# Performance work log

Measured on AMD Instinct MI355X. Metric: run time of the kernel, lower is better.

The kernel has to match this reference:

```python
import jax, jax.numpy as jnp
import numpy as np

N_HEADS = 16
D_MODEL = 1024
D_HEAD = D_MODEL // N_HEADS


def setup_inputs() -> dict:
    key = jax.random.key(0)
    k1, k2, k3, k4, k5 = jax.random.split(key, 5)
    B, S = 4, 2048
    scale = 1.0 / np.sqrt(D_MODEL)
    return {
        "x": jax.random.normal(k1, (B, S, D_MODEL), dtype=jnp.float32),
        "W_in": jax.random.normal(k2, (3 * D_MODEL, D_MODEL), dtype=jnp.float32) * scale,
        "b_in": jax.random.normal(k3, (3 * D_MODEL,), dtype=jnp.float32) * 0.02,
        "W_out": jax.random.normal(k4, (D_MODEL, D_MODEL), dtype=jnp.float32) * scale,
        "b_out": jax.random.normal(k5, (D_MODEL,), dtype=jnp.float32) * 0.02,
        "causal_mask": 1,
    }


def reference(x, W_in, b_in, W_out, b_out, causal_mask):
    b, s, d = x.shape
    # in_proj: torch Linear -> x @ W.T + b, then chunk into q,k,v
    qkv = jnp.einsum("bsd,ed->bse", x, W_in) + b_in
    q, k, v = jnp.split(qkv, 3, axis=-1)
    # [b, s, h, dh] -> [b, h, s, dh]
    q = q.reshape(b, s, N_HEADS, D_HEAD).transpose(0, 2, 1, 3)
    k = k.reshape(b, s, N_HEADS, D_HEAD).transpose(0, 2, 1, 3)
    v = v.reshape(b, s, N_HEADS, D_HEAD).transpose(0, 2, 1, 3)
    # scores [b, h, s, s]
    qk = jnp.einsum("bhqd,bhkd->bhqk", q, k)
    if causal_mask:
        mask = jnp.triu(jnp.ones((s, s), dtype=bool), k=1)
        qk = jnp.where(mask, -jnp.inf, qk)
    qk = qk / jnp.sqrt(jnp.float32(D_HEAD))
    attn = jax.nn.softmax(qk, axis=-1)
    out = jnp.einsum("bhqk,bhkd->bhqd", attn, v)  # [b, h, s, dh]
    out = out.transpose(0, 2, 1, 3).reshape(b, s, d)
    return jnp.einsum("bsd,ed->bse", out, W_out) + b_out
```

## Files before the change

### kernel.cpp

```cpp
#include <hip/hip_runtime.h>
#include <hip/hip_bf16.h>
#include <cstdint>
#include <cstddef>

typedef short bf16x8 __attribute__((ext_vector_type(8)));
typedef float f32x4 __attribute__((ext_vector_type(4)));

#define SEQ 2048
#define NH 16
#define DH 64
#define DM 1024

typedef __attribute__((address_space(1))) const void gvoid_t;
typedef __attribute__((address_space(3))) void lvoid_t;

__device__ __forceinline__ unsigned short f2bf(float f) {
  union { float f; unsigned int u; } v; v.f = f;
  return (unsigned short)((v.u + 0x7FFFu + ((v.u >> 16) & 1u)) >> 16);
}

__global__ void __launch_bounds__(256) k_cvt3(const float* __restrict__ x,
                                              const float* __restrict__ wi,
                                              const float* __restrict__ wo,
                                              unsigned short* __restrict__ xb,
                                              unsigned short* __restrict__ wib,
                                              unsigned short* __restrict__ wob) {
  int bidx = blockIdx.x;
  const float* src; unsigned short* dst; int base;
  if (bidx < 8192)       { src = x;  dst = xb;  base = bidx; }
  else if (bidx < 11264) { src = wi; dst = wib; base = bidx - 8192; }
  else                   { src = wo; dst = wob; base = bidx - 11264; }
  int i = (base * 256 + threadIdx.x) * 4;
  float4 v = *(const float4*)(src + i);
  ushort4 o;
  o.x = f2bf(v.x); o.y = f2bf(v.y); o.z = f2bf(v.z); o.w = f2bf(v.w);
  *(ushort4*)(dst + i) = o;
}

#define LDS_T 16384

__device__ __forceinline__ void barx() {
  asm volatile("" ::: "memory");
  __builtin_amdgcn_s_barrier();
  asm volatile("" ::: "memory");
}
#define LGKM0() asm volatile("s_waitcnt lgkmcnt(0)" ::: "memory")
#define VMC4()  asm volatile("s_waitcnt vmcnt(4)" ::: "memory")

__device__ __forceinline__ void stage_half(const unsigned short* __restrict__ G,
                                           int row0, int kt, unsigned short* lds,
                                           int Rhalf, int rstat, int cOff, int wave) {
#pragma unroll
  for (int pc = 0; pc < 2; ++pc) {
    const int R = Rhalf + pc * 64;
    __builtin_amdgcn_global_load_lds(
        (gvoid_t*)(G + (size_t)(row0 + R + rstat) * DM + kt * 64 + cOff),
        (lvoid_t*)(lds + (R + wave * 8) * 64), 16, 0, 0);
  }
}

__device__ __forceinline__ void lda8(const unsigned short* lds, int rb, int l16,
                                     int sw0, int sw1, bf16x8 (&a)[8]) {
#pragma unroll
  for (int f = 0; f < 4; ++f) {
    const unsigned short* p = lds + (rb + f * 16 + l16) * 64;
    a[f * 2 + 0] = *(const bf16x8*)(p + sw0);
    a[f * 2 + 1] = *(const bf16x8*)(p + sw1);
  }
}

__device__ __forceinline__ void ldb4(const unsigned short* lds, int rb, int l16,
                                     int sw0, int sw1, bf16x8 (&b)[4]) {
#pragma unroll
  for (int g = 0; g < 2; ++g) {
    const unsigned short* p = lds + (rb + g * 16 + l16) * 64;
    b[g * 2 + 0] = *(const bf16x8*)(p + sw0);
    b[g * 2 + 1] = *(const bf16x8*)(p + sw1);
  }
}

template <int MQ, int NQ>
__device__ __forceinline__ void mfma_quad(const bf16x8 (&a)[8], const bf16x8 (&b)[4],
                                          f32x4 (&acc)[8][4]) {
  __builtin_amdgcn_s_setprio(1);
#pragma unroll
  for (int f = 0; f < 4; ++f)
#pragma unroll
    for (int g = 0; g < 2; ++g) {
      f32x4 c = acc[MQ * 4 + f][NQ * 2 + g];
      c = __builtin_amdgcn_mfma_f32_16x16x32_bf16(a[f * 2 + 0], b[g * 2 + 0], c, 0, 0, 0);
      c = __builtin_amdgcn_mfma_f32_16x16x32_bf16(a[f * 2 + 1], b[g * 2 + 1], c, 0, 0, 0);
      acc[MQ * 4 + f][NQ * 2 + g] = c;
    }
  __builtin_amdgcn_s_setprio(0);
}

__device__ __forceinline__ void gemm256(const unsigned short* __restrict__ A,
                                        const unsigned short* __restrict__ Bt,
                                        unsigned short* lA, unsigned short* lB,
                                        int m0, int n0, f32x4 (&acc)[8][4]) {
  const int t = threadIdx.x;
  const int wave = t >> 6, lane = t & 63, quad = lane >> 4, l16 = lane & 15;
  const int wm = wave >> 2, wn = wave & 3;
  const int rstat = t >> 3;
  const int cOff = ((t & 7) ^ (rstat & 7)) * 8;
  const int sw0 = (quad ^ (l16 & 7)) * 8;
  const int sw1 = ((quad ^ 4) ^ (l16 & 7)) * 8;
  const int arb0 = wm * 64, arb1 = 128 + wm * 64;
  const int brb0 = wn * 32, brb1 = 128 + wn * 32;
  const int NT = DM / 64;

  bf16x8 af[8], b0[4], b1[4];

  stage_half(A,  m0, 0, lA, 0,   rstat, cOff, wave);
  stage_half(Bt, n0, 0, lB, 0,   rstat, cOff, wave);
  stage_half(A,  m0, 0, lA, 128, rstat, cOff, wave);
  stage_half(Bt, n0, 0, lB, 128, rstat, cOff, wave);
  stage_half(A,  m0, 1, lA + LDS_T, 0,   rstat, cOff, wave);
  stage_half(Bt, n0, 1, lB + LDS_T, 128, rstat, cOff, wave);
  VMC4();
  barx();

  for (int t0 = 0; t0 < NT; t0 += 2) {
    const int t2 = (t0 + 2 < NT) ? t0 + 2 : NT - 1;
    const int t3 = (t0 + 3 < NT) ? t0 + 3 : NT - 1;
    lda8(lA, arb0, l16, sw0, sw1, af);
    ldb4(lB, brb0, l16, sw0, sw1, b0);
    stage_half(A, m0, t0 + 1, lA + LDS_T, 128, rstat, cOff, wave);
    barx(); LGKM0();
    mfma_quad<0, 0>(af, b0, acc);
    barx();
    ldb4(lB, brb1, l16, sw0, sw1, b1);
    stage_half(Bt, n0, t0 + 1, lB + LDS_T, 0, rstat, cOff, wave);
    barx(); LGKM0();
    mfma_quad<0, 1>(af, b1, acc);
    barx();
    lda8(lA, arb1, l16, sw0, sw1, af);
    stage_half(A, m0, t2, lA, 0, rstat, cOff, wave);
    barx(); LGKM0();
    mfma_quad<1, 1>(af, b1, acc);
    barx();
    stage_half(Bt, n0, t2, lB, 128, rstat, cOff, wave);
    VMC4();
    barx(); LGKM0();
    mfma_quad<1, 0>(af, b0, acc);
    barx();
    lda8(lA + LDS_T, arb0, l16, sw0, sw1, af);
    ldb4(lB + LDS_T, brb0, l16, sw0, sw1, b0);
    stage_half(A, m0, t2, lA, 128, rstat, cOff, wave);
    barx(); LGKM0();
    mfma_quad<0, 0>(af, b0, acc);
    barx();
    ldb4(lB + LDS_T, brb1, l16, sw0, sw1, b1);
    stage_half(Bt, n0, t2, lB, 0, rstat, cOff, wave);
    barx(); LGKM0();
    mfma_quad<0, 1>(af, b1, acc);
    barx();
    lda8(lA + LDS_T, arb1, l16, sw0, sw1, af);
    stage_half(A, m0, t3, lA + LDS_T, 0, rstat, cOff, wave);
    barx(); LGKM0();
    mfma_quad<1, 1>(af, b1, acc);
    barx();
    stage_half(Bt, n0, t3, lB + LDS_T, 128, rstat, cOff, wave);
    VMC4();
    barx(); LGKM0();
    mfma_quad<1, 0>(af, b0, acc);
    barx();
  }
}

__global__ void __launch_bounds__(512, 2) k_gemm_qkv(
    const unsigned short* __restrict__ X,
    const unsigned short* __restrict__ Wi,
    const float* __restrict__ bias,
    unsigned short* __restrict__ Qo,
    unsigned short* __restrict__ Ko,
    unsigned short* __restrict__ Vto) {
  __shared__ unsigned short lA[2 * LDS_T];
  __shared__ unsigned short lB[2 * LDS_T];
  const int t = threadIdx.x;
  const int wave = t >> 6, lane = t & 63, quad = lane >> 4, l16 = lane & 15;
  const int wm = wave >> 2, wn = wave & 3;
  const int nwg = 32 * 12;
  const int bid = blockIdx.x;
  const int swz = (bid & 7) * (nwg / 8) + (bid >> 3);
  const int m0 = (swz / 12) * 256, n0 = (swz % 12) * 256;

  f32x4 acc[8][4];
  f32x4 zf = {0.f, 0.f, 0.f, 0.f};
#pragma unroll
  for (int i = 0; i < 8; ++i)
#pragma unroll
    for (int j = 0; j < 4; ++j) acc[i][j] = zf;

  gemm256(X, Wi, lA, lB, m0, n0, acc);

  const float SCALE = 0.18033688011112042f;
  const int sel = n0 >> 10;
#pragma unroll
  for (int nf = 0; nf < 4; ++nf) {
    const int gcol = n0 + (nf >> 1) * 128 + wn * 32 + (nf & 1) * 16 + l16;
    const float bv = bias[gcol];
    const int c = gcol & 1023;
    const int hh = c >> 6, dh = c & 63;
    if (sel == 0) {
#pragma unroll
      for (int mf = 0; mf < 8; ++mf) {
        const int grow = m0 + (mf >> 2) * 128 + wm * 64 + (mf & 3) * 16 + quad * 4;
        const int bb = grow >> 11, sb = grow & 2047;
        unsigned short* qp = Qo + ((size_t)(bb * NH + hh) * SEQ + sb) * DH + dh;
#pragma unroll
        for (int r = 0; r < 4; ++r)
          qp[(size_t)r * DH] = f2bf((acc[mf][nf][r] + bv) * SCALE);
      }
    } else if (sel == 1) {
#pragma unroll
      for (int mf = 0; mf < 8; ++mf) {
        const int grow = m0 + (mf >> 2) * 128 + wm * 64 + (mf & 3) * 16 + quad * 4;
        const int bb = grow >> 11, sb = grow & 2047;
        unsigned short* kp = Ko + ((size_t)(bb * NH + hh) * SEQ + sb) * DH + dh;
#pragma unroll
        for (int r = 0; r < 4; ++r)
          kp[(size_t)r * DH] = f2bf(acc[mf][nf][r] + bv);
      }
    } else {
#pragma unroll
      for (int mf = 0; mf < 8; ++mf) {
        const int grow = m0 + (mf >> 2) * 128 + wm * 64 + (mf & 3) * 16 + quad * 4;
        const int bb = grow >> 11, sb = grow & 2047;
        ushort4 pk;
        pk.x = f2bf(acc[mf][nf][0] + bv);
        pk.y = f2bf(acc[mf][nf][1] + bv);
        pk.z = f2bf(acc[mf][nf][2] + bv);
        pk.w = f2bf(acc[mf][nf][3] + bv);
        *(ushort4*)(&Vto[((size_t)(bb * NH + hh) * DH + dh) * SEQ + sb]) = pk;
      }
    }
  }
}

#define ASTR 72

__global__ void __launch_bounds__(256, 4) k_attn(
    const unsigned short* __restrict__ Q,
    const unsigned short* __restrict__ K,
    const unsigned short* __restrict__ Vt,
    unsigned short* __restrict__ Ao,
    const int* __restrict__ causal_p) {
  __shared__ unsigned short lK[64 * 64];
  __shared__ unsigned short lV[64 * 64];
  __shared__ unsigned short lP[2][4][16 * ASTR];

  const int t = threadIdx.x;
  const int wave = t >> 6, lane = t & 63, quad = lane >> 4, l16 = lane & 15;
  const int x = blockIdx.x, h = blockIdx.y, b = blockIdx.z;
  const int qtA = x, qtB = 31 - x;
  const int bh = b * NH + h;
  const int causal = causal_p[0];
  const int ktA = causal ? qtA : 31;
  const int ktB = causal ? qtB : 31;
  const int q0A = qtA * 64, q0B = qtB * 64;

  const unsigned short* Qb = Q + (size_t)bh * SEQ * DH;
  const unsigned short* Kb = K + (size_t)bh * SEQ * DH;
  const unsigned short* Vb = Vt + (size_t)bh * DH * SEQ;

  bf16x8 qA0 = *(const bf16x8*)(&Qb[(q0A + wave * 16 + l16) * DH + quad * 8]);
  bf16x8 qA1 = *(const bf16x8*)(&Qb[(q0A + wave * 16 + l16) * DH + 32 + quad * 8]);
  bf16x8 qB0 = *(const bf16x8*)(&Qb[(q0B + wave * 16 + l16) * DH + quad * 8]);
  bf16x8 qB1 = *(const bf16x8*)(&Qb[(q0B + wave * 16 + l16) * DH + 32 + quad * 8]);

  f32x4 zf = {0.f, 0.f, 0.f, 0.f};
  f32x4 oA[4], oB[4];
  for (int i = 0; i < 4; ++i) { oA[i] = zf; oB[i] = zf; }
  f32x4 lacA = zf, lacB = zf;

  bf16x8 ones;
#pragma unroll
  for (int i = 0; i < 8; ++i) ones[i] = (short)0x3F80;

  unsigned short* lPa = &lP[0][wave][0];
  unsigned short* lPb = &lP[1][wave][0];

  const int i0 = t, i1 = 256 + t;
  const int rr0 = i0 >> 3, cc0 = ((i0 & 7) ^ (rr0 & 7)) * 8;
  const int rr1 = i1 >> 3, cc1 = ((i1 & 7) ^ (rr1 & 7)) * 8;
  const int kof0 = rr0 * DH + cc0, kof1 = rr1 * DH + cc1;
  const int vof0 = rr0 * SEQ + cc0, vof1 = rr1 * SEQ + cc1;
  const int rbase = l16 * 64;
  const int sw0 = ((quad ^ (l16 & 7)) * 8);
  const int sw1 = (((quad ^ 4) ^ (l16 & 7)) * 8);

  for (int kt = 0; kt <= ktB; ++kt) {
    const int k0 = kt * 64;
    const bool doA = (kt <= ktA);

    __syncthreads();
    __builtin_amdgcn_global_load_lds((gvoid_t*)(Kb + (size_t)k0 * DH + kof0),
                                     (lvoid_t*)&lK[wave * 512], 16, 0, 0);
    __builtin_amdgcn_global_load_lds((gvoid_t*)(Kb + (size_t)k0 * DH + kof1),
                                     (lvoid_t*)&lK[wave * 512 + 2048], 16, 0, 0);
    __builtin_amdgcn_global_load_lds((gvoid_t*)(Vb + k0 + vof0),
                                     (lvoid_t*)&lV[wave * 512], 16, 0, 0);
    __builtin_amdgcn_global_load_lds((gvoid_t*)(Vb + k0 + vof1),
                                     (lvoid_t*)&lV[wave * 512 + 2048], 16, 0, 0);
    __syncthreads();

    f32x4 sA[4], sB[4];
#pragma unroll
    for (int nt = 0; nt < 4; ++nt) {
      bf16x8 kf0 = *(const bf16x8*)(&lK[nt * 1024 + rbase + sw0]);
      bf16x8 kf1 = *(const bf16x8*)(&lK[nt * 1024 + rbase + sw1]);
      f32x4 zb = zf;
      zb = __builtin_amdgcn_mfma_f32_16x16x32_bf16(qB0, kf0, zb, 0, 0, 0);
      zb = __builtin_amdgcn_mfma_f32_16x16x32_bf16(qB1, kf1, zb, 0, 0, 0);
      sB[nt] = zb;
      if (doA) {
        f32x4 za = zf;
        za = __builtin_amdgcn_mfma_f32_16x16x32_bf16(qA0, kf0, za, 0, 0, 0);
        za = __builtin_amdgcn_mfma_f32_16x16x32_bf16(qA1, kf1, za, 0, 0, 0);
        sA[nt] = za;
      }
    }

    if (causal && kt == qtB) {
#pragma unroll
      for (int nt = 0; nt < 4; ++nt) {
        int kcol = k0 + nt * 16 + l16;
#pragma unroll
        for (int r = 0; r < 4; ++r)
          if (kcol > q0B + wave * 16 + quad * 4 + r) sB[nt][r] = -1e30f;
      }
    }
    if (causal && doA && kt == qtA) {
#pragma unroll
      for (int nt = 0; nt < 4; ++nt) {
        int kcol = k0 + nt * 16 + l16;
#pragma unroll
        for (int r = 0; r < 4; ++r)
          if (kcol > q0A + wave * 16 + quad * 4 + r) sA[nt][r] = -1e30f;
      }
    }

#pragma unroll
    for (int nt = 0; nt < 4; ++nt)
#pragma unroll
      for (int r = 0; r < 4; ++r)
        lPb[(quad * 4 + r) * ASTR + nt * 16 + l16] =
            f2bf(__builtin_amdgcn_exp2f(sB[nt][r]));
    if (doA) {
#pragma unroll
      for (int nt = 0; nt < 4; ++nt)
#pragma unroll
        for (int r = 0; r < 4; ++r)
          lPa[(quad * 4 + r) * ASTR + nt * 16 + l16] =
              f2bf(__builtin_amdgcn_exp2f(sA[nt][r]));
    }

    asm volatile("s_waitcnt lgkmcnt(0)" ::: "memory");

    bf16x8 pB0 = *(const bf16x8*)(&lPb[l16 * ASTR + quad * 8]);
    bf16x8 pB1 = *(const bf16x8*)(&lPb[l16 * ASTR + 32 + quad * 8]);
    bf16x8 pA0 = pB0, pA1 = pB1;
    if (doA) {
      pA0 = *(const bf16x8*)(&lPa[l16 * ASTR + quad * 8]);
      pA1 = *(const bf16x8*)(&lPa[l16 * ASTR + 32 + quad * 8]);
    }

    lacB = __builtin_amdgcn_mfma_f32_16x16x32_bf16(pB0, ones, lacB, 0, 0, 0);
    lacB = __builtin_amdgcn_mfma_f32_16x16x32_bf16(pB1, ones, lacB, 0, 0, 0);
    if (doA) {
      lacA = __builtin_amdgcn_mfma_f32_16x16x32_bf16(pA0, ones, lacA, 0, 0, 0);
      lacA = __builtin_amdgcn_mfma_f32_16x16x32_bf16(pA1, ones, lacA, 0, 0, 0);
    }

#pragma unroll
    for (int nt = 0; nt < 4; ++nt) {
      bf16x8 vf0 = *(const bf16x8*)(&lV[nt * 1024 + rbase + sw0]);
      bf16x8 vf1 = *(const bf16x8*)(&lV[nt * 1024 + rbase + sw1]);
      oB[nt] = __builtin_amdgcn_mfma_f32_16x16x32_bf16(pB0, vf0, oB[nt], 0, 0, 0);
      oB[nt] = __builtin_amdgcn_mfma_f32_16x16x32_bf16(pB1, vf1, oB[nt], 0, 0, 0);
      if (doA) {
        oA[nt] = __builtin_amdgcn_mfma_f32_16x16x32_bf16(pA0, vf0, oA[nt], 0, 0, 0);
        oA[nt] = __builtin_amdgcn_mfma_f32_16x16x32_bf16(pA1, vf1, oA[nt], 0, 0, 0);
      }
    }
  }

#pragma unroll
  for (int r = 0; r < 4; ++r) {
    float invB = 1.0f / lacB[r];
    float invA = 1.0f / lacA[r];
#pragma unroll
    for (int nt = 0; nt < 4; ++nt) {
      int dh = nt * 16 + l16;
      int qgB = q0B + wave * 16 + quad * 4 + r;
      Ao[(size_t)(b * SEQ + qgB) * DM + h * DH + dh] = f2bf(oB[nt][r] * invB);
      int qgA = q0A + wave * 16 + quad * 4 + r;
      Ao[(size_t)(b * SEQ + qgA) * DM + h * DH + dh] = f2bf(oA[nt][r] * invA);
    }
  }
}

__global__ void __launch_bounds__(512, 2) k_gemm_out(
    const unsigned short* __restrict__ Ai,
    const unsigned short* __restrict__ Wo,
    const float* __restrict__ bias,
    float* __restrict__ C) {
  __shared__ unsigned short lA[2 * LDS_T];
  __shared__ unsigned short lB[2 * LDS_T];
  const int t = threadIdx.x;
  const int wave = t >> 6, lane = t & 63, quad = lane >> 4, l16 = lane & 15;
  const int wm = wave >> 2, wn = wave & 3;
  const int bid = blockIdx.x;
  const int swz = (bid & 7) * 16 + (bid >> 3);
  const int m0 = (swz >> 2) * 256, n0 = (swz & 3) * 256;

  f32x4 acc[8][4];
  f32x4 zf = {0.f, 0.f, 0.f, 0.f};
#pragma unroll
  for (int i = 0; i < 8; ++i)
#pragma unroll
    for (int j = 0; j < 4; ++j) acc[i][j] = zf;

  gemm256(Ai, Wo, lA, lB, m0, n0, acc);

#pragma unroll
  for (int nf = 0; nf < 4; ++nf) {
    const int gcol = n0 + (nf >> 1) * 128 + wn * 32 + (nf & 1) * 16 + l16;
    const float bv = bias[gcol];
#pragma unroll
    for (int mf = 0; mf < 8; ++mf) {
      const int grow = m0 + (mf >> 2) * 128 + wm * 64 + (mf & 3) * 16 + quad * 4;
#pragma unroll
      for (int r = 0; r < 4; ++r)
        C[(size_t)(grow + r) * DM + gcol] = acc[mf][nf][r] + bv;
    }
  }
}

extern "C" void kernel_launch(void* const* d_in, const int* in_sizes, int n_in,
                              void* d_out, int out_size, void* d_ws, size_t ws_size,
                              hipStream_t stream) {
  (void)in_sizes; (void)n_in; (void)out_size; (void)ws_size;
  const float* x     = (const float*)d_in[0];
  const float* W_in  = (const float*)d_in[1];
  const float* b_in  = (const float*)d_in[2];
  const float* W_out = (const float*)d_in[3];
  const float* b_out = (const float*)d_in[4];
  const int* causal  = (const int*)d_in[5];
  float* out = (float*)d_out;
  char* ws = (char*)d_ws;

  unsigned short* xb  = (unsigned short*)(ws + 0);
  unsigned short* Aob = (unsigned short*)(ws + 0);
  unsigned short* Wib = (unsigned short*)(ws + (size_t)(16 << 20));
  unsigned short* Wob = (unsigned short*)(ws + (size_t)(22 << 20));
  unsigned short* Qb  = (unsigned short*)(ws + (size_t)(24 << 20));
  unsigned short* Kb  = (unsigned short*)(ws + (size_t)(40 << 20));
  unsigned short* Vtb = (unsigned short*)(ws + (size_t)(56 << 20));

  k_cvt3<<<12288, 256, 0, stream>>>(x, W_in, W_out, xb, Wib, Wob);
  k_gemm_qkv<<<384, 512, 0, stream>>>(xb, Wib, b_in, Qb, Kb, Vtb);
  k_attn<<<dim3(16, 16, 4), 256, 0, stream>>>(Qb, Kb, Vtb, Aob, causal);
  k_gemm_out<<<128, 512, 0, stream>>>(Aob, Wob, b_out, out);
}
```

Baseline: 262.1 us.

## Double-buffer K/V tiles in attention and restructure GEMM staging with asm LDS reads

The attention kernel now double-buffers K and V tiles in LDS, prefetching the next tile with global_load_lds while the current one is computed. This replaces the two __syncthreads per iteration with a single vmcnt wait and barrier. The P buffer moves to a single XOR-swizzled per-wave layout written with ds_write_b16 and read with inline-asm ds_read_b128, so the A and B halves are processed in sequence through the same buffer. The GEMM mainloop reorders its staging sequence one half-tile earlier, uses vmcnt(6), adds sched_barrier fences around the MFMA blocks and switches LDS fragment reads to inline asm. The added explicit waits and scheduling fences risk serialising work the compiler could otherwise overlap.

```diff
diff --git a/kernel.cpp b/kernel.cpp
--- a/kernel.cpp
+++ b/kernel.cpp
@@ -13,11 +13,32 @@
 
 typedef __attribute__((address_space(1))) const void gvoid_t;
 typedef __attribute__((address_space(3))) void lvoid_t;
+typedef __attribute__((address_space(3))) const unsigned short ls_t;
 
 __device__ __forceinline__ unsigned short f2bf(float f) {
   union { float f; unsigned int u; } v; v.f = f;
   return (unsigned short)((v.u + 0x7FFFu + ((v.u >> 16) & 1u)) >> 16);
 }
+
+__device__ __forceinline__ bf16x8 dsr128(const unsigned short* p) {
+  bf16x8 r;
+  unsigned a = (unsigned)(size_t)(ls_t*)p;
+  asm volatile("ds_read_b128 %0, %1" : "=v"(r) : "v"(a));
+  return r;
+}
+__device__ __forceinline__ void dsw16(unsigned a, unsigned short v) {
+  asm volatile("ds_write_b16 %0, %1" :: "v"(a), "v"((unsigned)v));
+}
+
+__device__ __forceinline__ void barx() {
+  asm volatile("" ::: "memory");
+  __builtin_amdgcn_s_barrier();
+  asm volatile("" ::: "memory");
+}
+#define LGKM0() asm volatile("s_waitcnt lgkmcnt(0)" ::: "memory")
+#define VMC0()  asm volatile("s_waitcnt vmcnt(0)" ::: "memory")
+#define VMC6()  asm volatile("s_waitcnt vmcnt(6)" ::: "memory")
+#define SCHED0() __builtin_amdgcn_sched_barrier(0)
 
 __global__ void __launch_bounds__(256) k_cvt3(const float* __restrict__ x,
                                               const float* __restrict__ wi,
@@ -39,14 +60,6 @@
 
 #define LDS_T 16384
 
-__device__ __forceinline__ void barx() {
-  asm volatile("" ::: "memory");
-  __builtin_amdgcn_s_barrier();
-  asm volatile("" ::: "memory");
-}
-#define LGKM0() asm volatile("s_waitcnt lgkmcnt(0)" ::: "memory")
-#define VMC4()  asm volatile("s_waitcnt vmcnt(4)" ::: "memory")
-
 __device__ __forceinline__ void stage_half(const unsigned short* __restrict__ G,
                                            int row0, int kt, unsigned short* lds,
                                            int Rhalf, int rstat, int cOff, int wave) {
@@ -59,23 +72,23 @@
   }
 }
 
-__device__ __forceinline__ void lda8(const unsigned short* lds, int rb, int l16,
-                                     int sw0, int sw1, bf16x8 (&a)[8]) {
+__device__ __forceinline__ void lda8a(const unsigned short* lds, int rb, int l16,
+                                      int sw0, int sw1, bf16x8 (&a)[8]) {
 #pragma unroll
   for (int f = 0; f < 4; ++f) {
     const unsigned short* p = lds + (rb + f * 16 + l16) * 64;
-    a[f * 2 + 0] = *(const bf16x8*)(p + sw0);
-    a[f * 2 + 1] = *(const bf16x8*)(p + sw1);
-  }
-}
-
-__device__ __forceinline__ void ldb4(const unsigned short* lds, int rb, int l16,
-                                     int sw0, int sw1, bf16x8 (&b)[4]) {
+    a[f * 2 + 0] = dsr128(p + sw0);
+    a[f * 2 + 1] = dsr128(p + sw1);
+  }
+}
+
+__device__ __forceinline__ void ldb4a(const unsigned short* lds, int rb, int l16,
+                                      int sw0, int sw1, bf16x8 (&b)[4]) {
 #pragma unroll
   for (int g = 0; g < 2; ++g) {
     const unsigned short* p = lds + (rb + g * 16 + l16) * 64;
-    b[g * 2 + 0] = *(const bf16x8*)(p + sw0);
-    b[g * 2 + 1] = *(const bf16x8*)(p + sw1);
+    b[g * 2 + 0] = dsr128(p + sw0);
+    b[g * 2 + 1] = dsr128(p + sw1);
   }
 }
 
@@ -118,54 +131,55 @@
   stage_half(Bt, n0, 0, lB, 128, rstat, cOff, wave);
   stage_half(A,  m0, 1, lA + LDS_T, 0,   rstat, cOff, wave);
   stage_half(Bt, n0, 1, lB + LDS_T, 128, rstat, cOff, wave);
-  VMC4();
+  stage_half(A,  m0, 1, lA + LDS_T, 128, rstat, cOff, wave);
+  VMC6();
   barx();
 
   for (int t0 = 0; t0 < NT; t0 += 2) {
     const int t2 = (t0 + 2 < NT) ? t0 + 2 : NT - 1;
     const int t3 = (t0 + 3 < NT) ? t0 + 3 : NT - 1;
-    lda8(lA, arb0, l16, sw0, sw1, af);
-    ldb4(lB, brb0, l16, sw0, sw1, b0);
-    stage_half(A, m0, t0 + 1, lA + LDS_T, 128, rstat, cOff, wave);
-    barx(); LGKM0();
+    lda8a(lA, arb0, l16, sw0, sw1, af);
+    ldb4a(lB, brb0, l16, sw0, sw1, b0);
+    stage_half(Bt, n0, t0 + 1, lB + LDS_T, 0, rstat, cOff, wave);
+    barx(); LGKM0(); SCHED0();
     mfma_quad<0, 0>(af, b0, acc);
-    barx();
-    ldb4(lB, brb1, l16, sw0, sw1, b1);
-    stage_half(Bt, n0, t0 + 1, lB + LDS_T, 0, rstat, cOff, wave);
-    barx(); LGKM0();
+    SCHED0(); barx();
+    ldb4a(lB, brb1, l16, sw0, sw1, b1);
+    stage_half(A, m0, t2, lA, 0, rstat, cOff, wave);
+    barx(); LGKM0(); SCHED0();
     mfma_quad<0, 1>(af, b1, acc);
-    barx();
-    lda8(lA, arb1, l16, sw0, sw1, af);
-    stage_half(A, m0, t2, lA, 0, rstat, cOff, wave);
-    barx(); LGKM0();
+    SCHED0(); barx();
+    lda8a(lA, arb1, l16, sw0, sw1, af);
+    stage_half(Bt, n0, t2, lB, 128, rstat, cOff, wave);
+    barx(); LGKM0(); SCHED0();
     mfma_quad<1, 1>(af, b1, acc);
-    barx();
-    stage_half(Bt, n0, t2, lB, 128, rstat, cOff, wave);
-    VMC4();
-    barx(); LGKM0();
+    SCHED0(); barx();
+    stage_half(A, m0, t2, lA, 128, rstat, cOff, wave);
+    VMC6();
+    barx(); SCHED0();
     mfma_quad<1, 0>(af, b0, acc);
-    barx();
-    lda8(lA + LDS_T, arb0, l16, sw0, sw1, af);
-    ldb4(lB + LDS_T, brb0, l16, sw0, sw1, b0);
-    stage_half(A, m0, t2, lA, 128, rstat, cOff, wave);
-    barx(); LGKM0();
+    SCHED0(); barx();
+    lda8a(lA + LDS_T, arb0, l16, sw0, sw1, af);
+    ldb4a(lB + LDS_T, brb0, l16, sw0, sw1, b0);
+    stage_half(Bt, n0, t2, lB, 0, rstat, cOff, wave);
+    barx(); LGKM0(); SCHED0();
     mfma_quad<0, 0>(af, b0, acc);
-    barx();
-    ldb4(lB + LDS_T, brb1, l16, sw0, sw1, b1);
-    stage_half(Bt, n0, t2, lB, 0, rstat, cOff, wave);
-    barx(); LGKM0();
+    SCHED0(); barx();
+    ldb4a(lB + LDS_T, brb1, l16, sw0, sw1, b1);
+    stage_half(A, m0, t3, lA + LDS_T, 0, rstat, cOff, wave);
+    barx(); LGKM0(); SCHED0();
     mfma_quad<0, 1>(af, b1, acc);
-    barx();
-    lda8(lA + LDS_T, arb1, l16, sw0, sw1, af);
-    stage_half(A, m0, t3, lA + LDS_T, 0, rstat, cOff, wave);
-    barx(); LGKM0();
+    SCHED0(); barx();
+    lda8a(lA + LDS_T, arb1, l16, sw0, sw1, af);
+    stage_half(Bt, n0, t3, lB + LDS_T, 128, rstat, cOff, wave);
+    barx(); LGKM0(); SCHED0();
     mfma_quad<1, 1>(af, b1, acc);
-    barx();
-    stage_half(Bt, n0, t3, lB + LDS_T, 128, rstat, cOff, wave);
-    VMC4();
-    barx(); LGKM0();
+    SCHED0(); barx();
+    stage_half(A, m0, t3, lA + LDS_T, 128, rstat, cOff, wave);
+    VMC6();
+    barx(); SCHED0();
     mfma_quad<1, 0>(af, b0, acc);
-    barx();
+    SCHED0(); barx();
   }
 }
 
@@ -239,17 +253,15 @@
   }
 }
 
-#define ASTR 72
-
 __global__ void __launch_bounds__(256, 4) k_attn(
     const unsigned short* __restrict__ Q,
     const unsigned short* __restrict__ K,
     const unsigned short* __restrict__ Vt,
     unsigned short* __restrict__ Ao,
     const int* __restrict__ causal_p) {
-  __shared__ unsigned short lK[64 * 64];
-  __shared__ unsigned short lV[64 * 64];
-  __shared__ unsigned short lP[2][4][16 * ASTR];
+  __shared__ unsigned short lK[2][4096];
+  __shared__ unsigned short lV[2][4096];
+  __shared__ unsigned short lP[4][1024];
 
   const int t = threadIdx.x;
   const int wave = t >> 6, lane = t & 63, quad = lane >> 4, l16 = lane & 15;
@@ -279,8 +291,8 @@
 #pragma unroll
   for (int i = 0; i < 8; ++i) ones[i] = (short)0x3F80;
 
-  unsigned short* lPa = &lP[0][wave][0];
-  unsigned short* lPb = &lP[1][wave][0];
+  unsigned short* lPw = &lP[wave][0];
+  const unsigned pbase = (unsigned)(size_t)(ls_t*)lPw;
 
   const int i0 = t, i1 = 256 + t;
   const int rr0 = i0 >> 3, cc0 = ((i0 & 7) ^ (rr0 & 7)) * 8;
@@ -291,35 +303,56 @@
   const int sw0 = ((quad ^ (l16 & 7)) * 8);
   const int sw1 = (((quad ^ 4) ^ (l16 & 7)) * 8);
 
+  __builtin_amdgcn_global_load_lds((gvoid_t*)(Kb + kof0), (lvoid_t*)&lK[0][wave * 512], 16, 0, 0);
+  __builtin_amdgcn_global_load_lds((gvoid_t*)(Kb + kof1), (lvoid_t*)&lK[0][wave * 512 + 2048], 16, 0, 0);
+  __builtin_amdgcn_global_load_lds((gvoid_t*)(Vb + vof0), (lvoid_t*)&lV[0][wave * 512], 16, 0, 0);
+  __builtin_amdgcn_global_load_lds((gvoid_t*)(Vb + vof1), (lvoid_t*)&lV[0][wave * 512 + 2048], 16, 0, 0);
+
   for (int kt = 0; kt <= ktB; ++kt) {
+    const int cur = kt & 1;
     const int k0 = kt * 64;
     const bool doA = (kt <= ktA);
 
-    __syncthreads();
-    __builtin_amdgcn_global_load_lds((gvoid_t*)(Kb + (size_t)k0 * DH + kof0),
-                                     (lvoid_t*)&lK[wave * 512], 16, 0, 0);
-    __builtin_amdgcn_global_load_lds((gvoid_t*)(Kb + (size_t)k0 * DH + kof1),
-                                     (lvoid_t*)&lK[wave * 512 + 2048], 16, 0, 0);
-    __builtin_amdgcn_global_load_lds((gvoid_t*)(Vb + k0 + vof0),
-                                     (lvoid_t*)&lV[wave * 512], 16, 0, 0);
-    __builtin_amdgcn_global_load_lds((gvoid_t*)(Vb + k0 + vof1),
-                                     (lvoid_t*)&lV[wave * 512 + 2048], 16, 0, 0);
-    __syncthreads();
+    VMC0();
+    barx();
+    if (kt < ktB) {
+      const int kn = k0 + 64;
+      __builtin_amdgcn_global_load_lds((gvoid_t*)(Kb + (size_t)kn * DH + kof0),
+                                       (lvoid_t*)&lK[cur ^ 1][wave * 512], 16, 0, 0);
+      __builtin_amdgcn_global_load_lds((gvoid_t*)(Kb + (size_t)kn * DH + kof1),
+                                       (lvoid_t*)&lK[cur ^ 1][wave * 512 + 2048], 16, 0, 0);
+      __builtin_amdgcn_global_load_lds((gvoid_t*)(Vb + kn + vof0),
+                                       (lvoid_t*)&lV[cur ^ 1][wave * 512], 16, 0, 0);
+      __builtin_amdgcn_global_load_lds((gvoid_t*)(Vb + kn + vof1),
+                                       (lvoid_t*)&lV[cur ^ 1][wave * 512 + 2048], 16, 0, 0);
+    }
+    const unsigned short* lk = &lK[cur][0];
+    const unsigned short* lv = &lV[cur][0];
 
     f32x4 sA[4], sB[4];
 #pragma unroll
-    for (int nt = 0; nt < 4; ++nt) {
-      bf16x8 kf0 = *(const bf16x8*)(&lK[nt * 1024 + rbase + sw0]);
-      bf16x8 kf1 = *(const bf16x8*)(&lK[nt * 1024 + rbase + sw1]);
-      f32x4 zb = zf;
-      zb = __builtin_amdgcn_mfma_f32_16x16x32_bf16(qB0, kf0, zb, 0, 0, 0);
-      zb = __builtin_amdgcn_mfma_f32_16x16x32_bf16(qB1, kf1, zb, 0, 0, 0);
-      sB[nt] = zb;
-      if (doA) {
-        f32x4 za = zf;
-        za = __builtin_amdgcn_mfma_f32_16x16x32_bf16(qA0, kf0, za, 0, 0, 0);
-        za = __builtin_amdgcn_mfma_f32_16x16x32_bf16(qA1, kf1, za, 0, 0, 0);
-        sA[nt] = za;
+    for (int g = 0; g < 2; ++g) {
+      bf16x8 kf[4];
+#pragma unroll
+      for (int j = 0; j < 2; ++j) {
+        const unsigned short* p = lk + (g * 2 + j) * 1024 + rbase;
+        kf[j * 2 + 0] = dsr128(p + sw0);
+        kf[j * 2 + 1] = dsr128(p + sw1);
+      }
+      LGKM0(); SCHED0();
+#pragma unroll
+      for (int j = 0; j < 2; ++j) {
+        const int nt = g * 2 + j;
+        f32x4 zb = zf;
+        zb = __builtin_amdgcn_mfma_f32_16x16x32_bf16(qB0, kf[j * 2 + 0], zb, 0, 0, 0);
+        zb = __builtin_amdgcn_mfma_f32_16x16x32_bf16(qB1, kf[j * 2 + 1], zb, 0, 0, 0);
+        sB[nt] = zb;
+        if (doA) {
+          f32x4 za = zf;
+          za = __builtin_amdgcn_mfma_f32_16x16x32_bf16(qA0, kf[j * 2 + 0], za, 0, 0, 0);
+          za = __builtin_amdgcn_mfma_f32_16x16x32_bf16(qA1, kf[j * 2 + 1], za, 0, 0, 0);
+          sA[nt] = za;
+        }
       }
     }
 
@@ -345,45 +378,59 @@
 #pragma unroll
     for (int nt = 0; nt < 4; ++nt)
 #pragma unroll
-      for (int r = 0; r < 4; ++r)
-        lPb[(quad * 4 + r) * ASTR + nt * 16 + l16] =
-            f2bf(__builtin_amdgcn_exp2f(sB[nt][r]));
-    if (doA) {
-#pragma unroll
-      for (int nt = 0; nt < 4; ++nt)
-#pragma unroll
-        for (int r = 0; r < 4; ++r)
-          lPa[(quad * 4 + r) * ASTR + nt * 16 + l16] =
-              f2bf(__builtin_amdgcn_exp2f(sA[nt][r]));
-    }
-
-    asm volatile("s_waitcnt lgkmcnt(0)" ::: "memory");
-
-    bf16x8 pB0 = *(const bf16x8*)(&lPb[l16 * ASTR + quad * 8]);
-    bf16x8 pB1 = *(const bf16x8*)(&lPb[l16 * ASTR + 32 + quad * 8]);
+      for (int r = 0; r < 4; ++r) {
+        const int row = quad * 4 + r;
+        const unsigned a = pbase +
+            (unsigned)(row * 64 + (((nt * 2 + (l16 >> 3)) ^ (row & 7)) * 8) + (l16 & 7)) * 2u;
+        dsw16(a, f2bf(__builtin_amdgcn_exp2f(sB[nt][r])));
+      }
+    LGKM0(); SCHED0();
+    bf16x8 pB0 = dsr128(lPw + rbase + sw0);
+    bf16x8 pB1 = dsr128(lPw + rbase + sw1);
+    LGKM0(); SCHED0();
+    lacB = __builtin_amdgcn_mfma_f32_16x16x32_bf16(pB0, ones, lacB, 0, 0, 0);
+    lacB = __builtin_amdgcn_mfma_f32_16x16x32_bf16(pB1, ones, lacB, 0, 0, 0);
+
     bf16x8 pA0 = pB0, pA1 = pB1;
     if (doA) {
-      pA0 = *(const bf16x8*)(&lPa[l16 * ASTR + quad * 8]);
-      pA1 = *(const bf16x8*)(&lPa[l16 * ASTR + 32 + quad * 8]);
-    }
-
-    lacB = __builtin_amdgcn_mfma_f32_16x16x32_bf16(pB0, ones, lacB, 0, 0, 0);
-    lacB = __builtin_amdgcn_mfma_f32_16x16x32_bf16(pB1, ones, lacB, 0, 0, 0);
-    if (doA) {
+#pragma unroll
+      for (int nt = 0; nt < 4; ++nt)
+#pragma unroll
+        for (int r = 0; r < 4; ++r) {
+          const int row = quad * 4 + r;
+          const unsigned a = pbase +
+              (unsigned)(row * 64 + (((nt * 2 + (l16 >> 3)) ^ (row & 7)) * 8) + (l16 & 7)) * 2u;
+          dsw16(a, f2bf(__builtin_amdgcn_exp2f(sA[nt][r])));
+        }
+      LGKM0(); SCHED0();
+      pA0 = dsr128(lPw + rbase + sw0);
+      pA1 = dsr128(lPw + rbase + sw1);
+      LGKM0(); SCHED0();
       lacA = __builtin_amdgcn_mfma_f32_16x16x32_bf16(pA0, ones, lacA, 0, 0, 0);
       lacA = __builtin_amdgcn_mfma_f32_16x16x32_bf16(pA1, ones, lacA, 0, 0, 0);
     }
 
 #pragma unroll
-    for (int nt = 0; nt < 4; ++nt) {
-      bf16x8 vf0 = *(const bf16x8*)(&lV[nt * 1024 + rbase + sw0]);
-      bf16x8 vf1 = *(const bf16x8*)(&lV[nt * 1024 + rbase + sw1]);
-      oB[nt] = __builtin_amdgcn_mfma_f32_16x16x32_bf16(pB0, vf0, oB[nt], 0, 0, 0);
-      oB[nt] = __builtin_amdgcn_mfma_f32_16x16x32_bf16(pB1, vf1, oB[nt], 0, 0, 0);
-      if (doA) {
-        oA[nt] = __builtin_amdgcn_mfma_f32_16x16x32_bf16(pA0, vf0, oA[nt], 0, 0, 0);
-        oA[nt] = __builtin_amdgcn_mfma_f32_16x16x32_bf16(pA1, vf1, oA[nt], 0, 0, 0);
-      }
+    for (int g = 0; g < 2; ++g) {
+      bf16x8 vf[4];
+#pragma unroll
+      for (int j = 0; j < 2; ++j) {
+        const unsigned short* p = lv + (g * 2 + j) * 1024 + rbase;
+        vf[j * 2 + 0] = dsr128(p + sw0);
+        vf[j * 2 + 1] = dsr128(p + sw1);
+      }
+      LGKM0(); SCHED0();
+#pragma unroll
+      for (int j = 0; j < 2; ++j) {
+        const int nt = g * 2 + j;
+        oB[nt] = __builtin_amdgcn_mfma_f32_16x16x32_bf16(pB0, vf[j * 2 + 0], oB[nt], 0, 0, 0);
+        oB[nt] = __builtin_amdgcn_mfma_f32_16x16x32_bf16(pB1, vf[j * 2 + 1], oB[nt], 0, 0, 0);
+        if (doA) {
+          oA[nt] = __builtin_amdgcn_mfma_f32_16x16x32_bf16(pA0, vf[j * 2 + 0], oA[nt], 0, 0, 0);
+          oA[nt] = __builtin_amdgcn_mfma_f32_16x16x32_bf16(pA1, vf[j * 2 + 1], oA[nt], 0, 0, 0);
+        }
+      }
+      SCHED0();
     }
   }
 
```

Result: slower. 282.8 us (+7.9%).

## Restructure GEMMs to 128x256 tiles with B operand held in registers

Applied to the files above, without the earlier changes.

Both projection GEMMs switch from 256x256 LDS-staged A and B tiles to 128x256 tiles. Only A is staged through LDS with double buffering, and each wave loads its B fragments straight from global memory into registers, with inline ds_read_b128 and sched barriers. This doubles the grid size to improve CU occupancy and cuts LDS traffic, at the cost of redundant global reads of B and less reuse per tile. The attention launch also becomes 1D with an XCD-aware remap of block ids to heads.

```diff
diff --git a/kernel.cpp b/kernel.cpp
--- a/kernel.cpp
+++ b/kernel.cpp
@@ -13,11 +13,29 @@
 
 typedef __attribute__((address_space(1))) const void gvoid_t;
 typedef __attribute__((address_space(3))) void lvoid_t;
+typedef __attribute__((address_space(3))) const unsigned short ls_t;
 
 __device__ __forceinline__ unsigned short f2bf(float f) {
   union { float f; unsigned int u; } v; v.f = f;
   return (unsigned short)((v.u + 0x7FFFu + ((v.u >> 16) & 1u)) >> 16);
 }
+
+__device__ __forceinline__ bf16x8 dsr128(const unsigned short* p) {
+  bf16x8 r;
+  unsigned a = (unsigned)(size_t)(ls_t*)p;
+  asm volatile("ds_read_b128 %0, %1" : "=v"(r) : "v"(a));
+  return r;
+}
+
+__device__ __forceinline__ void barx() {
+  asm volatile("" ::: "memory");
+  __builtin_amdgcn_s_barrier();
+  asm volatile("" ::: "memory");
+}
+#define LGKM0()  asm volatile("s_waitcnt lgkmcnt(0)" ::: "memory")
+#define VMC8()   asm volatile("s_waitcnt vmcnt(8)" ::: "memory")
+#define SCHED0() __builtin_amdgcn_sched_barrier(0)
+#define SFENCE() asm volatile("" ::: "memory")
 
 __global__ void __launch_bounds__(256) k_cvt3(const float* __restrict__ x,
                                               const float* __restrict__ wi,
@@ -37,134 +55,90 @@
   *(ushort4*)(dst + i) = o;
 }
 
-#define LDS_T 16384
-
-__device__ __forceinline__ void barx() {
-  asm volatile("" ::: "memory");
-  __builtin_amdgcn_s_barrier();
-  asm volatile("" ::: "memory");
-}
-#define LGKM0() asm volatile("s_waitcnt lgkmcnt(0)" ::: "memory")
-#define VMC4()  asm volatile("s_waitcnt vmcnt(4)" ::: "memory")
-
-__device__ __forceinline__ void stage_half(const unsigned short* __restrict__ G,
-                                           int row0, int kt, unsigned short* lds,
-                                           int Rhalf, int rstat, int cOff, int wave) {
-#pragma unroll
-  for (int pc = 0; pc < 2; ++pc) {
-    const int R = Rhalf + pc * 64;
+template <int NLD>
+__device__ __forceinline__ void stageA(const unsigned short* __restrict__ G, int m0,
+                                       int kt, unsigned short* lds, int t) {
+#pragma unroll
+  for (int r = 0; r < NLD; ++r) {
+    const int i = r * 512 + t;
+    const int row = i >> 3;
+    const int c = ((i & 7) ^ (row & 7)) * 8;
     __builtin_amdgcn_global_load_lds(
-        (gvoid_t*)(G + (size_t)(row0 + R + rstat) * DM + kt * 64 + cOff),
-        (lvoid_t*)(lds + (R + wave * 8) * 64), 16, 0, 0);
-  }
-}
-
-__device__ __forceinline__ void lda8(const unsigned short* lds, int rb, int l16,
-                                     int sw0, int sw1, bf16x8 (&a)[8]) {
-#pragma unroll
-  for (int f = 0; f < 4; ++f) {
-    const unsigned short* p = lds + (rb + f * 16 + l16) * 64;
-    a[f * 2 + 0] = *(const bf16x8*)(p + sw0);
-    a[f * 2 + 1] = *(const bf16x8*)(p + sw1);
-  }
-}
-
-__device__ __forceinline__ void ldb4(const unsigned short* lds, int rb, int l16,
-                                     int sw0, int sw1, bf16x8 (&b)[4]) {
-#pragma unroll
-  for (int g = 0; g < 2; ++g) {
-    const unsigned short* p = lds + (rb + g * 16 + l16) * 64;
-    b[g * 2 + 0] = *(const bf16x8*)(p + sw0);
-    b[g * 2 + 1] = *(const bf16x8*)(p + sw1);
-  }
-}
-
-template <int MQ, int NQ>
-__device__ __forceinline__ void mfma_quad(const bf16x8 (&a)[8], const bf16x8 (&b)[4],
-                                          f32x4 (&acc)[8][4]) {
-  __builtin_amdgcn_s_setprio(1);
-#pragma unroll
-  for (int f = 0; f < 4; ++f)
-#pragma unroll
-    for (int g = 0; g < 2; ++g) {
-      f32x4 c = acc[MQ * 4 + f][NQ * 2 + g];
-      c = __builtin_amdgcn_mfma_f32_16x16x32_bf16(a[f * 2 + 0], b[g * 2 + 0], c, 0, 0, 0);
-      c = __builtin_amdgcn_mfma_f32_16x16x32_bf16(a[f * 2 + 1], b[g * 2 + 1], c, 0, 0, 0);
-      acc[MQ * 4 + f][NQ * 2 + g] = c;
-    }
-  __builtin_amdgcn_s_setprio(0);
-}
-
-__device__ __forceinline__ void gemm256(const unsigned short* __restrict__ A,
-                                        const unsigned short* __restrict__ Bt,
-                                        unsigned short* lA, unsigned short* lB,
-                                        int m0, int n0, f32x4 (&acc)[8][4]) {
+        (gvoid_t*)(G + (size_t)(m0 + row) * DM + kt * 64 + c),
+        (lvoid_t*)(lds + i * 8), 16, 0, 0);
+  }
+}
+
+__device__ __forceinline__ void loadB(bf16x8 (&b)[8], const unsigned short* bp, int kt) {
+  const int k0 = kt * 64;
+#pragma unroll
+  for (int nf = 0; nf < 4; ++nf)
+#pragma unroll
+    for (int h = 0; h < 2; ++h)
+      b[nf * 2 + h] = *(const bf16x8*)(bp + (size_t)nf * 16 * DM + k0 + h * 32);
+}
+
+template <int MF>
+__device__ __forceinline__ void computeK(const unsigned short* lbuf, int wmrow0,
+                                         int l16, int sw0, int sw1,
+                                         const bf16x8 (&b)[8], f32x4 (&acc)[MF][4]) {
+#pragma unroll
+  for (int q = 0; q < MF / 4; ++q) {
+    bf16x8 af[8];
+#pragma unroll
+    for (int f = 0; f < 4; ++f) {
+      const unsigned short* p = lbuf + (wmrow0 + (q * 4 + f) * 16 + l16) * 64;
+      af[f * 2 + 0] = dsr128(p + sw0);
+      af[f * 2 + 1] = dsr128(p + sw1);
+    }
+    LGKM0(); SCHED0();
+    __builtin_amdgcn_s_setprio(1);
+#pragma unroll
+    for (int f = 0; f < 4; ++f)
+#pragma unroll
+      for (int nf = 0; nf < 4; ++nf) {
+        f32x4 c = acc[q * 4 + f][nf];
+        c = __builtin_amdgcn_mfma_f32_16x16x32_bf16(af[f * 2 + 0], b[nf * 2 + 0], c, 0, 0, 0);
+        c = __builtin_amdgcn_mfma_f32_16x16x32_bf16(af[f * 2 + 1], b[nf * 2 + 1], c, 0, 0, 0);
+        acc[q * 4 + f][nf] = c;
+      }
+    __builtin_amdgcn_s_setprio(0);
+  }
+}
+
+template <int MF>
+__device__ __forceinline__ void gemm_breg(const unsigned short* __restrict__ A,
+                                          const unsigned short* __restrict__ Bt,
+                                          unsigned short* lds, int m0, int n0,
+                                          f32x4 (&acc)[MF][4]) {
+  constexpr int NLD = MF / 2;
+  constexpr int TILE = MF * 32 * 64;
   const int t = threadIdx.x;
-  const int wave = t >> 6, lane = t & 63, quad = lane >> 4, l16 = lane & 15;
+  const int lane = t & 63, quad = (t & 63) >> 4, l16 = t & 15;
+  const int wave = t >> 6;
   const int wm = wave >> 2, wn = wave & 3;
-  const int rstat = t >> 3;
-  const int cOff = ((t & 7) ^ (rstat & 7)) * 8;
+  (void)lane;
   const int sw0 = (quad ^ (l16 & 7)) * 8;
   const int sw1 = ((quad ^ 4) ^ (l16 & 7)) * 8;
-  const int arb0 = wm * 64, arb1 = 128 + wm * 64;
-  const int brb0 = wn * 32, brb1 = 128 + wn * 32;
-  const int NT = DM / 64;
-
-  bf16x8 af[8], b0[4], b1[4];
-
-  stage_half(A,  m0, 0, lA, 0,   rstat, cOff, wave);
-  stage_half(Bt, n0, 0, lB, 0,   rstat, cOff, wave);
-  stage_half(A,  m0, 0, lA, 128, rstat, cOff, wave);
-  stage_half(Bt, n0, 0, lB, 128, rstat, cOff, wave);
-  stage_half(A,  m0, 1, lA + LDS_T, 0,   rstat, cOff, wave);
-  stage_half(Bt, n0, 1, lB + LDS_T, 128, rstat, cOff, wave);
-  VMC4();
-  barx();
-
-  for (int t0 = 0; t0 < NT; t0 += 2) {
-    const int t2 = (t0 + 2 < NT) ? t0 + 2 : NT - 1;
-    const int t3 = (t0 + 3 < NT) ? t0 + 3 : NT - 1;
-    lda8(lA, arb0, l16, sw0, sw1, af);
-    ldb4(lB, brb0, l16, sw0, sw1, b0);
-    stage_half(A, m0, t0 + 1, lA + LDS_T, 128, rstat, cOff, wave);
-    barx(); LGKM0();
-    mfma_quad<0, 0>(af, b0, acc);
+  const int wmrow0 = wm * MF * 16;
+  const unsigned short* bp = Bt + (size_t)(n0 + wn * 64 + l16) * DM + quad * 8;
+
+  bf16x8 b0[8], b1[8];
+  stageA<NLD>(A, m0, 0, lds, t);
+  SFENCE();
+  loadB(b0, bp, 0);
+  VMC8(); barx();
+
+  for (int t0 = 0; t0 < 16; t0 += 2) {
+    stageA<NLD>(A, m0, t0 + 1, lds + TILE, t);
+    SFENCE();
+    computeK<MF>(lds, wmrow0, l16, sw0, sw1, b0, acc);
+    loadB(b1, bp, t0 + 1);
+    VMC8();
     barx();
-    ldb4(lB, brb1, l16, sw0, sw1, b1);
-    stage_half(Bt, n0, t0 + 1, lB + LDS_T, 0, rstat, cOff, wave);
-    barx(); LGKM0();
-    mfma_quad<0, 1>(af, b1, acc);
-    barx();
-    lda8(lA, arb1, l16, sw0, sw1, af);
-    stage_half(A, m0, t2, lA, 0, rstat, cOff, wave);
-    barx(); LGKM0();
-    mfma_quad<1, 1>(af, b1, acc);
-    barx();
-    stage_half(Bt, n0, t2, lB, 128, rstat, cOff, wave);
-    VMC4();
-    barx(); LGKM0();
-    mfma_quad<1, 0>(af, b0, acc);
-    barx();
-    lda8(lA + LDS_T, arb0, l16, sw0, sw1, af);
-    ldb4(lB + LDS_T, brb0, l16, sw0, sw1, b0);
-    stage_half(A, m0, t2, lA, 128, rstat, cOff, wave);
-    barx(); LGKM0();
-    mfma_quad<0, 0>(af, b0, acc);
-    barx();
-    ldb4(lB + LDS_T, brb1, l16, sw0, sw1, b1);
-    stage_half(Bt, n0, t2, lB, 0, rstat, cOff, wave);
-    barx(); LGKM0();
-    mfma_quad<0, 1>(af, b1, acc);
-    barx();
-    lda8(lA + LDS_T, arb1, l16, sw0, sw1, af);
-    stage_half(A, m0, t3, lA + LDS_T, 0, rstat, cOff, wave);
-    barx(); LGKM0();
-    mfma_quad<1, 1>(af, b1, acc);
-    barx();
-    stage_half(Bt, n0, t3, lB + LDS_T, 128, rstat, cOff, wave);
-    VMC4();
-    barx(); LGKM0();
-    mfma_quad<1, 0>(af, b0, acc);
+    if (t0 + 2 < 16) { stageA<NLD>(A, m0, t0 + 2, lds, t); SFENCE(); }
+    computeK<MF>(lds + TILE, wmrow0, l16, sw0, sw1, b1, acc);
+    if (t0 + 2 < 16) { loadB(b0, bp, t0 + 2); VMC8(); }
     barx();
   }
 }
@@ -176,37 +150,35 @@
     unsigned short* __restrict__ Qo,
     unsigned short* __restrict__ Ko,
     unsigned short* __restrict__ Vto) {
-  __shared__ unsigned short lA[2 * LDS_T];
-  __shared__ unsigned short lB[2 * LDS_T];
+  __shared__ unsigned short lds[2 * 128 * 64];
   const int t = threadIdx.x;
   const int wave = t >> 6, lane = t & 63, quad = lane >> 4, l16 = lane & 15;
   const int wm = wave >> 2, wn = wave & 3;
-  const int nwg = 32 * 12;
   const int bid = blockIdx.x;
-  const int swz = (bid & 7) * (nwg / 8) + (bid >> 3);
-  const int m0 = (swz / 12) * 256, n0 = (swz % 12) * 256;
-
-  f32x4 acc[8][4];
+  const int swz = (bid & 7) * 96 + (bid >> 3);
+  const int n0 = (swz >> 6) * 256, m0 = (swz & 63) * 128;
+
+  f32x4 acc[4][4];
   f32x4 zf = {0.f, 0.f, 0.f, 0.f};
 #pragma unroll
-  for (int i = 0; i < 8; ++i)
+  for (int i = 0; i < 4; ++i)
 #pragma unroll
     for (int j = 0; j < 4; ++j) acc[i][j] = zf;
 
-  gemm256(X, Wi, lA, lB, m0, n0, acc);
+  gemm_breg<4>(X, Wi, lds, m0, n0, acc);
 
   const float SCALE = 0.18033688011112042f;
   const int sel = n0 >> 10;
 #pragma unroll
   for (int nf = 0; nf < 4; ++nf) {
-    const int gcol = n0 + (nf >> 1) * 128 + wn * 32 + (nf & 1) * 16 + l16;
+    const int gcol = n0 + wn * 64 + nf * 16 + l16;
     const float bv = bias[gcol];
     const int c = gcol & 1023;
     const int hh = c >> 6, dh = c & 63;
     if (sel == 0) {
 #pragma unroll
-      for (int mf = 0; mf < 8; ++mf) {
-        const int grow = m0 + (mf >> 2) * 128 + wm * 64 + (mf & 3) * 16 + quad * 4;
+      for (int mf = 0; mf < 4; ++mf) {
+        const int grow = m0 + wm * 64 + mf * 16 + quad * 4;
         const int bb = grow >> 11, sb = grow & 2047;
         unsigned short* qp = Qo + ((size_t)(bb * NH + hh) * SEQ + sb) * DH + dh;
 #pragma unroll
@@ -215,8 +187,8 @@
       }
     } else if (sel == 1) {
 #pragma unroll
-      for (int mf = 0; mf < 8; ++mf) {
-        const int grow = m0 + (mf >> 2) * 128 + wm * 64 + (mf & 3) * 16 + quad * 4;
+      for (int mf = 0; mf < 4; ++mf) {
+        const int grow = m0 + wm * 64 + mf * 16 + quad * 4;
         const int bb = grow >> 11, sb = grow & 2047;
         unsigned short* kp = Ko + ((size_t)(bb * NH + hh) * SEQ + sb) * DH + dh;
 #pragma unroll
@@ -225,8 +197,8 @@
       }
     } else {
 #pragma unroll
-      for (int mf = 0; mf < 8; ++mf) {
-        const int grow = m0 + (mf >> 2) * 128 + wm * 64 + (mf & 3) * 16 + quad * 4;
+      for (int mf = 0; mf < 4; ++mf) {
+        const int grow = m0 + wm * 64 + mf * 16 + quad * 4;
         const int bb = grow >> 11, sb = grow & 2047;
         ushort4 pk;
         pk.x = f2bf(acc[mf][nf][0] + bv);
@@ -253,7 +225,10 @@
 
   const int t = threadIdx.x;
   const int wave = t >> 6, lane = t & 63, quad = lane >> 4, l16 = lane & 15;
-  const int x = blockIdx.x, h = blockIdx.y, b = blockIdx.z;
+  const int id = blockIdx.x;
+  const int cxcd = id & 7, w = id >> 3;
+  const int x = w & 15, g = (w >> 4) * 8 + cxcd;
+  const int h = g & 15, b = g >> 4;
   const int qtA = x, qtB = 31 - x;
   const int bh = b * NH + h;
   const int causal = causal_p[0];
@@ -407,31 +382,30 @@
     const unsigned short* __restrict__ Wo,
     const float* __restrict__ bias,
     float* __restrict__ C) {
-  __shared__ unsigned short lA[2 * LDS_T];
-  __shared__ unsigned short lB[2 * LDS_T];
+  __shared__ unsigned short lds[2 * 128 * 64];
   const int t = threadIdx.x;
   const int wave = t >> 6, lane = t & 63, quad = lane >> 4, l16 = lane & 15;
   const int wm = wave >> 2, wn = wave & 3;
   const int bid = blockIdx.x;
-  const int swz = (bid & 7) * 16 + (bid >> 3);
-  const int m0 = (swz >> 2) * 256, n0 = (swz & 3) * 256;
-
-  f32x4 acc[8][4];
+  const int swz = (bid & 7) * 32 + (bid >> 3);
+  const int n0 = (swz >> 6) * 256, m0 = (swz & 63) * 128;
+
+  f32x4 acc[4][4];
   f32x4 zf = {0.f, 0.f, 0.f, 0.f};
 #pragma unroll
-  for (int i = 0; i < 8; ++i)
+  for (int i = 0; i < 4; ++i)
 #pragma unroll
     for (int j = 0; j < 4; ++j) acc[i][j] = zf;
 
-  gemm256(Ai, Wo, lA, lB, m0, n0, acc);
+  gemm_breg<4>(Ai, Wo, lds, m0, n0, acc);
 
 #pragma unroll
   for (int nf = 0; nf < 4; ++nf) {
-    const int gcol = n0 + (nf >> 1) * 128 + wn * 32 + (nf & 1) * 16 + l16;
+    const int gcol = n0 + wn * 64 + nf * 16 + l16;
     const float bv = bias[gcol];
 #pragma unroll
-    for (int mf = 0; mf < 8; ++mf) {
-      const int grow = m0 + (mf >> 2) * 128 + wm * 64 + (mf & 3) * 16 + quad * 4;
+    for (int mf = 0; mf < 4; ++mf) {
+      const int grow = m0 + wm * 64 + mf * 16 + quad * 4;
 #pragma unroll
       for (int r = 0; r < 4; ++r)
         C[(size_t)(grow + r) * DM + gcol] = acc[mf][nf][r] + bv;
@@ -461,7 +435,7 @@
   unsigned short* Vtb = (unsigned short*)(ws + (size_t)(56 << 20));
 
   k_cvt3<<<12288, 256, 0, stream>>>(x, W_in, W_out, xb, Wib, Wob);
-  k_gemm_qkv<<<384, 512, 0, stream>>>(xb, Wib, b_in, Qb, Kb, Vtb);
-  k_attn<<<dim3(16, 16, 4), 256, 0, stream>>>(Qb, Kb, Vtb, Aob, causal);
-  k_gemm_out<<<128, 512, 0, stream>>>(Aob, Wob, b_out, out);
-}
+  k_gemm_qkv<<<768, 512, 0, stream>>>(xb, Wib, b_in, Qb, Kb, Vtb);
+  k_attn<<<1024, 256, 0, stream>>>(Qb, Kb, Vtb, Aob, causal);
+  k_gemm_out<<<256, 512, 0, stream>>>(Aob, Wob, b_out, out);
+}
```

After: 329.6 us. 1.26x slower.
